# Kernel optimization log

Hardware: AMD Instinct MI355X
Metric: run time of the kernel (lower is better)

The kernel has to match this reference:

```python
import jax, jax.numpy as jnp
import numpy as np

T, H, E, I = 512, 2048, 8, 4096
W_SCALE = 0.02  # keep activations numerically sane with randn weights


def setup_inputs() -> dict:
    key = jax.random.key(0)
    k_x, k_r, k_w1, k_w3, k_w2 = jax.random.split(key, 5)
    x = jax.random.normal(k_x, (T, H), dtype=jnp.float32)
    router_logits = jax.random.normal(k_r, (T, E), dtype=jnp.float32)
    w1 = jax.random.normal(k_w1, (E, I, H), dtype=jnp.float32) * W_SCALE  # gate proj (silu branch)
    w3 = jax.random.normal(k_w3, (E, I, H), dtype=jnp.float32) * W_SCALE  # up proj
    w2 = jax.random.normal(k_w2, (E, H, I), dtype=jnp.float32) * W_SCALE  # down proj
    return {"x": x, "router_logits": router_logits, "w1": w1, "w3": w3, "w2": w2}


def reference(x, router_logits, w1, w3, w2):
    # Llama4 routing: top-1 expert, router weight = sigmoid(top logit),
    # applied on the INPUT (apply_router_weight_on_input=True).
    top_logit = jnp.max(router_logits, axis=-1)          # [T]
    expert_idx = jnp.argmax(router_logits, axis=-1)      # [T] int
    scale = jax.nn.sigmoid(top_logit)                    # [T]
    xs = x * scale[:, None]                              # [T, H]

    # Grouped SwiGLU experts (dense over E, combined with one-hot select;
    # faithful to fused grouped-GEMM math of FusedMoE).
    gate = jnp.einsum('th,eih->eti', xs, w1)             # [E, T, I]
    up = jnp.einsum('th,eih->eti', xs, w3)               # [E, T, I]
    h = jax.nn.silu(gate) * up                           # [E, T, I]
    y = jnp.einsum('eti,ehi->eth', h, w2)                # [E, T, H]

    onehot = jax.nn.one_hot(expert_idx, E, dtype=x.dtype)  # [T, E]
    out = jnp.einsum('te,eth->th', onehot, y)            # [T, H]
    return out
```

## Files before the change

kernel.cpp:

```cpp
#include <hip/hip_runtime.h>

#define T_TOK 512
#define HDIM 2048
#define NEXP 8
#define IDIM 4096

#define BM 128
#define BK 64
#define G1_BN 32
#define G2_BN 16

typedef float f32x4 __attribute__((ext_vector_type(4)));
typedef __bf16 bf16x8 __attribute__((ext_vector_type(8)));
typedef unsigned short ushort8 __attribute__((ext_vector_type(8)));

static __device__ __forceinline__ unsigned short f2bf(float f) {
    unsigned int u = __float_as_uint(f);
    u = (u + 0x7fffu + ((u >> 16) & 1u)) >> 16;
    return (unsigned short)u;
}

static __device__ __forceinline__ void gload_lds16(const void* g, void* l) {
    auto gp = reinterpret_cast<const unsigned int __attribute__((address_space(1)))*>(
        reinterpret_cast<unsigned long long>(g));
    auto lp = reinterpret_cast<unsigned int __attribute__((address_space(3)))*>(
        static_cast<unsigned int>(reinterpret_cast<unsigned long long>(l)));
    __builtin_amdgcn_global_load_lds(gp, lp, 16, 0, 0);
}

__global__ void k_route(const float* __restrict__ logits,
                        int* __restrict__ off, int* __restrict__ tok,
                        float* __restrict__ scale) {
    __shared__ int cnt[NEXP], cur[NEXP];
    const int t = threadIdx.x;
    if (t < NEXP) cnt[t] = 0;
    __syncthreads();
    float m = logits[t * NEXP];
    int a = 0;
#pragma unroll
    for (int j = 1; j < NEXP; ++j) {
        float v = logits[t * NEXP + j];
        if (v > m) { m = v; a = j; }
    }
    scale[t] = 1.f / (1.f + __expf(-m));
    atomicAdd(&cnt[a], 1);
    __syncthreads();
    if (t == 0) {
        int o = 0;
        for (int e = 0; e < NEXP; ++e) { off[e] = o; cur[e] = o; o += cnt[e]; }
        off[NEXP] = o;
    }
    __syncthreads();
    int r = atomicAdd(&cur[a], 1);
    tok[r] = t;
}

__global__ void k_gather(const float* __restrict__ x, const int* __restrict__ tok,
                         const float* __restrict__ scale,
                         unsigned short* __restrict__ xs) {
    const int pos = blockIdx.x;
    const int t = tok[pos];
    const float s = scale[t];
    const int c = threadIdx.x * 8;
    const float4* src = (const float4*)(x + (size_t)t * HDIM + c);
    float4 v0 = src[0], v1 = src[1];
    ushort8 o;
    o[0] = f2bf(v0.x * s); o[1] = f2bf(v0.y * s);
    o[2] = f2bf(v0.z * s); o[3] = f2bf(v0.w * s);
    o[4] = f2bf(v1.x * s); o[5] = f2bf(v1.y * s);
    o[6] = f2bf(v1.z * s); o[7] = f2bf(v1.w * s);
    *(ushort8*)(xs + (size_t)pos * HDIM + c) = o;
}

__global__ void __launch_bounds__(256, 2)
k_moe1(const unsigned short* __restrict__ xs,
       const float* __restrict__ w1,
       const float* __restrict__ w3,
       const int* __restrict__ off,
       unsigned short* __restrict__ hbuf) {
    __shared__ char smem[65536];

    const int tid = threadIdx.x;
    const int w = tid >> 6, l = tid & 63;
    const int e = blockIdx.x >> 7;
    const int n0 = (blockIdx.x & 127) * G1_BN;
    const int pos_beg = off[e], pos_end = off[e + 1];

    const char* bw1 = (const char*)(w1 + (size_t)e * IDIM * HDIM + (size_t)n0 * HDIM);
    const char* bw3 = (const char*)(w3 + (size_t)e * IDIM * HDIM + (size_t)n0 * HDIM);

    const int a_row = w * 8 + (l >> 3);
    const int a_cb  = ((l & 7) ^ (l >> 3)) << 4;
    const int b_row = w * 4 + (l >> 4);
    const int b_cb  = ((l & 15) << 4) ^ (((w * 4 + (l >> 4)) & 7) << 5);

    for (int m0 = pos_beg; m0 < pos_end; m0 += BM) {
        f32x4 zero = {0.f, 0.f, 0.f, 0.f};
        f32x4 accG[2][2], accU[2][2];
#pragma unroll
        for (int i = 0; i < 2; ++i)
#pragma unroll
            for (int j = 0; j < 2; ++j) { accG[i][j] = zero; accU[i][j] = zero; }

        auto stage = [&](int buf, int ks) {
            const int k0 = ks * BK;
#pragma unroll
            for (int j = 0; j < 4; ++j) {
                const int o = buf * 16384 + j * 4096 + w * 1024;
                int gr = m0 + j * 32 + a_row; gr = gr < T_TOK ? gr : T_TOK - 1;
                gload_lds16((const char*)xs + (size_t)gr * (HDIM * 2) + k0 * 2 + a_cb,
                            smem + o);
            }
#pragma unroll
            for (int j = 0; j < 2; ++j) {
                const size_t roff = (size_t)(j * 16 + b_row) * (HDIM * 4) + k0 * 4 + b_cb;
                gload_lds16(bw1 + roff, smem + 32768 + buf * 8192 + j * 4096 + w * 1024);
                gload_lds16(bw3 + roff, smem + 49152 + buf * 8192 + j * 4096 + w * 1024);
            }
        };

        stage(0, 0);
        asm volatile("s_waitcnt vmcnt(0)" ::: "memory");
        __syncthreads();

#pragma unroll 1
        for (int ks = 0; ks < HDIM / BK; ++ks) {
            const int cb = ks & 1;
            if (ks + 1 < HDIM / BK) stage(cb ^ 1, ks + 1);

            const char* cA  = smem + cb * 16384;
            const char* cB1 = smem + 32768 + cb * 8192;
            const char* cB3 = smem + 49152 + cb * 8192;
#pragma unroll
            for (int kk = 0; kk < 2; ++kk) {
                bf16x8 a[2];
#pragma unroll
                for (int fm = 0; fm < 2; ++fm) {
                    const int row = w * 32 + fm * 16 + (l & 15);
                    const int kb = (kk * 64 + ((l >> 4) << 4)) ^ ((l & 7) << 4);
                    a[fm] = *(const bf16x8*)(cA + row * 128 + kb);
                }
#pragma unroll
                for (int fn = 0; fn < 2; ++fn) {
                    const int row = fn * 16 + (l & 15);
                    const int kb = (kk * 128 + ((l >> 4) << 5)) ^ ((l & 7) << 5);
                    const char* p1 = cB1 + row * 256 + kb;
                    const char* p3 = cB3 + row * 256 + kb;
                    f32x4 g0 = *(const f32x4*)p1, g1 = *(const f32x4*)(p1 + 16);
                    f32x4 u0 = *(const f32x4*)p3, u1 = *(const f32x4*)(p3 + 16);
                    bf16x8 bg, bu;
#pragma unroll
                    for (int q = 0; q < 4; ++q) {
                        bg[q] = (__bf16)g0[q]; bg[q + 4] = (__bf16)g1[q];
                        bu[q] = (__bf16)u0[q]; bu[q + 4] = (__bf16)u1[q];
                    }
#pragma unroll
                    for (int fm = 0; fm < 2; ++fm) {
                        accG[fm][fn] = __builtin_amdgcn_mfma_f32_16x16x32_bf16(
                            a[fm], bg, accG[fm][fn], 0, 0, 0);
                        accU[fm][fn] = __builtin_amdgcn_mfma_f32_16x16x32_bf16(
                            a[fm], bu, accU[fm][fn], 0, 0, 0);
                    }
                }
            }
            asm volatile("s_waitcnt vmcnt(0)" ::: "memory");
            __syncthreads();
        }

#pragma unroll
        for (int fm = 0; fm < 2; ++fm)
#pragma unroll
            for (int fn = 0; fn < 2; ++fn)
#pragma unroll
                for (int r = 0; r < 4; ++r) {
                    const int pos = m0 + w * 32 + fm * 16 + ((l >> 4) << 2) + r;
                    if (pos < pos_end) {
                        const float gv = accG[fm][fn][r];
                        const float uv = accU[fm][fn][r];
                        const float hv = gv / (1.f + __expf(-gv)) * uv;
                        hbuf[(size_t)pos * IDIM + n0 + fn * 16 + (l & 15)] = f2bf(hv);
                    }
                }
    }
}

__global__ void __launch_bounds__(256, 4)
k_moe2(const unsigned short* __restrict__ hbuf,
       const float* __restrict__ w2,
       const int* __restrict__ off,
       const int* __restrict__ tok,
       float* __restrict__ out) {
    __shared__ char smem[40960];

    const int tid = threadIdx.x;
    const int w = tid >> 6, l = tid & 63;
    const int e = blockIdx.x >> 7;
    const int n0 = (blockIdx.x & 127) * G2_BN;
    const int pos_beg = off[e], pos_end = off[e + 1];
    const char* bw2 = (const char*)(w2 + (size_t)e * HDIM * IDIM + (size_t)n0 * IDIM);

    const int a_row = w * 8 + (l >> 3);
    const int a_cb  = ((l & 7) ^ (l >> 3)) << 4;
    const int b_row = w * 4 + (l >> 4);
    const int b_cb  = ((l & 15) << 4) ^ (((w * 4 + (l >> 4)) & 7) << 5);

    for (int m0 = pos_beg; m0 < pos_end; m0 += BM) {
        f32x4 zero = {0.f, 0.f, 0.f, 0.f};
        f32x4 acc[2];
        acc[0] = zero; acc[1] = zero;

        auto stage = [&](int buf, int ks) {
            const int k0 = ks * BK;
#pragma unroll
            for (int j = 0; j < 4; ++j) {
                const int o = buf * 16384 + j * 4096 + w * 1024;
                int gr = m0 + j * 32 + a_row; gr = gr < T_TOK ? gr : T_TOK - 1;
                gload_lds16((const char*)hbuf + (size_t)gr * (IDIM * 2) + k0 * 2 + a_cb,
                            smem + o);
            }
            gload_lds16(bw2 + (size_t)b_row * (IDIM * 4) + k0 * 4 + b_cb,
                        smem + 32768 + buf * 4096 + w * 1024);
        };

        stage(0, 0);
        asm volatile("s_waitcnt vmcnt(0)" ::: "memory");
        __syncthreads();

#pragma unroll 1
        for (int ks = 0; ks < IDIM / BK; ++ks) {
            const int cb = ks & 1;
            if (ks + 1 < IDIM / BK) stage(cb ^ 1, ks + 1);

            const char* cA = smem + cb * 16384;
            const char* cB = smem + 32768 + cb * 4096;
#pragma unroll
            for (int kk = 0; kk < 2; ++kk) {
                const int brow = l & 15;
                const int bkb = (kk * 128 + ((l >> 4) << 5)) ^ ((l & 7) << 5);
                const char* pb = cB + brow * 256 + bkb;
                f32x4 b0 = *(const f32x4*)pb, b1 = *(const f32x4*)(pb + 16);
                bf16x8 bb;
#pragma unroll
                for (int q = 0; q < 4; ++q) {
                    bb[q] = (__bf16)b0[q]; bb[q + 4] = (__bf16)b1[q];
                }
#pragma unroll
                for (int fm = 0; fm < 2; ++fm) {
                    const int row = w * 32 + fm * 16 + (l & 15);
                    const int kb = (kk * 64 + ((l >> 4) << 4)) ^ ((l & 7) << 4);
                    bf16x8 a = *(const bf16x8*)(cA + row * 128 + kb);
                    acc[fm] = __builtin_amdgcn_mfma_f32_16x16x32_bf16(a, bb, acc[fm], 0, 0, 0);
                }
            }
            asm volatile("s_waitcnt vmcnt(0)" ::: "memory");
            __syncthreads();
        }

#pragma unroll
        for (int fm = 0; fm < 2; ++fm)
#pragma unroll
            for (int r = 0; r < 4; ++r) {
                const int pos = m0 + w * 32 + fm * 16 + ((l >> 4) << 2) + r;
                if (pos < pos_end) {
                    const int t = tok[pos];
                    out[(size_t)t * HDIM + n0 + (l & 15)] = acc[fm][r];
                }
            }
    }
}

extern "C" void kernel_launch(void* const* d_in, const int* in_sizes, int n_in,
                              void* d_out, int out_size, void* d_ws, size_t ws_size,
                              hipStream_t stream) {
    const float* x      = (const float*)d_in[0];
    const float* logits = (const float*)d_in[1];
    const float* w1     = (const float*)d_in[2];
    const float* w3     = (const float*)d_in[3];
    const float* w2     = (const float*)d_in[4];
    float* out = (float*)d_out;

    char* ws = (char*)d_ws;
    int* off   = (int*)ws;
    int* tok   = (int*)(ws + 64);
    float* scl = (float*)(ws + 64 + 2048);
    unsigned short* xs   = (unsigned short*)(ws + 8192);
    unsigned short* hbuf = (unsigned short*)(ws + 8192 + (size_t)T_TOK * HDIM * 2);

    k_route<<<1, T_TOK, 0, stream>>>(logits, off, tok, scl);
    k_gather<<<T_TOK, 256, 0, stream>>>(x, tok, scl, xs);
    k_moe1<<<NEXP * (IDIM / G1_BN), 256, 0, stream>>>(xs, w1, w3, off, hbuf);
    k_moe2<<<NEXP * (HDIM / G2_BN), 256, 0, stream>>>(hbuf, w2, off, tok, out);
}
```

Before: 218.8 us.

## Deepen async LDS prefetch to two stages in flight with partial vmcnt waits

Both expert GEMM kernels now issue the global-to-LDS loads for the next two K tiles up front. Each iteration waits with a partial vmcnt, so only the older stage must have landed, and it refills the buffer just consumed after a barrier. This keeps one tile's loads in flight while the current tile computes, instead of draining all outstanding loads every step. In exchange each iteration needs two barriers, and it relies on hand-set vmcnt counts (8 and 5) that match the number of loads per stage.

```diff
diff --git a/kernel.cpp b/kernel.cpp
--- a/kernel.cpp
+++ b/kernel.cpp
@@ -79,6 +79,7 @@
        const int* __restrict__ off,
        unsigned short* __restrict__ hbuf) {
     __shared__ char smem[65536];
+    const int NK = HDIM / BK;
 
     const int tid = threadIdx.x;
     const int w = tid >> 6, l = tid & 63;
@@ -119,15 +120,15 @@
             }
         };
 
+        asm volatile("s_waitcnt vmcnt(0)" ::: "memory");
         stage(0, 0);
-        asm volatile("s_waitcnt vmcnt(0)" ::: "memory");
-        __syncthreads();
+        stage(1, 1);
+        asm volatile("s_waitcnt vmcnt(8)" ::: "memory");
+        __builtin_amdgcn_s_barrier();
 
 #pragma unroll 1
-        for (int ks = 0; ks < HDIM / BK; ++ks) {
+        for (int ks = 0; ks < NK; ++ks) {
             const int cb = ks & 1;
-            if (ks + 1 < HDIM / BK) stage(cb ^ 1, ks + 1);
-
             const char* cA  = smem + cb * 16384;
             const char* cB1 = smem + 32768 + cb * 8192;
             const char* cB3 = smem + 49152 + cb * 8192;
@@ -163,8 +164,18 @@
                     }
                 }
             }
-            asm volatile("s_waitcnt vmcnt(0)" ::: "memory");
-            __syncthreads();
+            asm volatile("s_waitcnt lgkmcnt(0)" ::: "memory");
+            __builtin_amdgcn_sched_barrier(0);
+            __builtin_amdgcn_s_barrier();
+            if (ks + 1 < NK) {
+                if (ks + 2 < NK) {
+                    stage(cb, ks + 2);
+                    asm volatile("s_waitcnt vmcnt(8)" ::: "memory");
+                } else {
+                    asm volatile("s_waitcnt vmcnt(0)" ::: "memory");
+                }
+                __builtin_amdgcn_s_barrier();
+            }
         }
 
 #pragma unroll
@@ -191,6 +202,7 @@
        const int* __restrict__ tok,
        float* __restrict__ out) {
     __shared__ char smem[40960];
+    const int NK = IDIM / BK;
 
     const int tid = threadIdx.x;
     const int w = tid >> 6, l = tid & 63;
@@ -222,15 +234,15 @@
                         smem + 32768 + buf * 4096 + w * 1024);
         };
 
+        asm volatile("s_waitcnt vmcnt(0)" ::: "memory");
         stage(0, 0);
-        asm volatile("s_waitcnt vmcnt(0)" ::: "memory");
-        __syncthreads();
+        stage(1, 1);
+        asm volatile("s_waitcnt vmcnt(5)" ::: "memory");
+        __builtin_amdgcn_s_barrier();
 
 #pragma unroll 1
-        for (int ks = 0; ks < IDIM / BK; ++ks) {
+        for (int ks = 0; ks < NK; ++ks) {
             const int cb = ks & 1;
-            if (ks + 1 < IDIM / BK) stage(cb ^ 1, ks + 1);
-
             const char* cA = smem + cb * 16384;
             const char* cB = smem + 32768 + cb * 4096;
 #pragma unroll
@@ -252,8 +264,18 @@
                     acc[fm] = __builtin_amdgcn_mfma_f32_16x16x32_bf16(a, bb, acc[fm], 0, 0, 0);
                 }
             }
-            asm volatile("s_waitcnt vmcnt(0)" ::: "memory");
-            __syncthreads();
+            asm volatile("s_waitcnt lgkmcnt(0)" ::: "memory");
+            __builtin_amdgcn_sched_barrier(0);
+            __builtin_amdgcn_s_barrier();
+            if (ks + 1 < NK) {
+                if (ks + 2 < NK) {
+                    stage(cb, ks + 2);
+                    asm volatile("s_waitcnt vmcnt(5)" ::: "memory");
+                } else {
+                    asm volatile("s_waitcnt vmcnt(0)" ::: "memory");
+                }
+                __builtin_amdgcn_s_barrier();
+            }
         }
 
 #pragma unroll
```

New measurement: 228.8 us. 4.6% more time.
